# Kernel optimization log

Measured on AMD Instinct MI355X. Metric: run time of the kernel, lower is better.

## Reference

```python
import jax, jax.numpy as jnp
import numpy as np
from jax import lax

DES_R = 2.0                      # descriptor radius (KITTI config)
RAD_N, ELE_N, AZI_N = 9, 40, 80  # spherical voxel grid
VOXEL_R = 0.3                    # per-voxel ball-query radius
NSAMPLE = 30                     # points kept per voxel
B, N = 2, 1024                   # patches, points per patch
M = RAD_N * ELE_N * AZI_N        # 28800 voxel centers
EPS = 1e-5                       # BatchNorm eps


def voxel_centers():
    # cm.get_voxel_coordinate: spherical grid, flatten order (rad, ele, azi)
    r = (np.arange(RAD_N) + 0.5) * DES_R / RAD_N
    ele = (np.arange(ELE_N) + 0.5) * np.pi / ELE_N
    azi = (np.arange(AZI_N) + 0.5) * 2.0 * np.pi / AZI_N
    rr, ee, aa = np.meshgrid(r, ele, azi, indexing='ij')
    x = rr * np.sin(ee) * np.cos(aa)
    y = rr * np.sin(ee) * np.sin(aa)
    z = rr * np.cos(ee)
    return jnp.asarray(np.stack([x, y, z], -1).reshape(-1, 3), jnp.float32)


def bn(x, g, b, axes):
    # train-mode BatchNorm (batch statistics), channel axis = 1
    m = x.mean(axes, keepdims=True)
    v = x.var(axes, keepdims=True)
    shape = [1] * x.ndim
    shape[1] = -1
    return g.reshape(shape) * (x - m) * lax.rsqrt(v + EPS) + b.reshape(shape)


def conv3d_cyl(x, w, b):
    # cylindrical 3D conv: valid over rad, zero-pad elevation, circular-pad azimuth
    xp = jnp.pad(x, ((0, 0), (0, 0), (0, 0), (1, 1), (0, 0)))
    xp = jnp.pad(xp, ((0, 0), (0, 0), (0, 0), (0, 0), (1, 1)), mode='wrap')
    y = lax.conv_general_dilated(xp, w, (1, 1, 1), 'VALID',
                                 dimension_numbers=('NCDHW', 'OIDHW', 'NCDHW'))
    return y + b[None, :, None, None, None]


def _forward(points, w_raise, b_raise, g0, be0,
             w1, b1, g1, be1, w2, b2, g2, be2,
             w3, b3, g3, be3, w4, b4, g4, be4):
    vox = voxel_centers()                               # (M,3)
    center = points[:, -1:, :]
    delta = points - center                             # (B,N,3), KITTI: no z-axis alignment

    # --- cm.sphere_query: fixed-radius ball query per voxel center ---
    d2 = (jnp.sum(delta * delta, -1)[:, None, :]
          + jnp.sum(vox * vox, -1)[None, :, None]
          - 2.0 * jnp.einsum('bnc,mc->bmn', delta, vox))   # (B,M,N)
    arange = jnp.arange(N, dtype=jnp.int32)
    idx_m = jnp.where(d2 <= VOXEL_R ** 2, arange[None, None, :], N)
    neg_small, _ = lax.top_k(-idx_m, NSAMPLE)           # smallest indices first
    idx = -neg_small                                    # (B,M,NSAMPLE)
    mask = idx == N                                     # empty slots -> voxel center
    gathered = jax.vmap(lambda d, i: d[i])(delta, jnp.where(mask, 0, idx))  # (B,M,ns,3)
    rel = jnp.where(mask[..., None], 0.0, gathered - vox[None, :, None, :])

    # --- cm.var_to_invar: undo each azimuth bin's rotation about z ---
    ang = -jnp.arange(AZI_N, dtype=jnp.float32) * jnp.float32(2.0 * np.pi / AZI_N)
    c, s = jnp.cos(ang), jnp.sin(ang)
    z0, o1 = jnp.zeros_like(c), jnp.ones_like(c)
    R = jnp.stack([jnp.stack([c, -s, z0], -1),
                   jnp.stack([s, c, z0], -1),
                   jnp.stack([z0, z0, o1], -1)], -2)     # (AZI_N,3,3)
    relv = rel.reshape(B, RAD_N, ELE_N, AZI_N, NSAMPLE, 3)
    relv = jnp.einsum('breanc,acd->breand', relv, R).reshape(B, M, NSAMPLE, 3)

    # --- xyz raising (1x1 conv) + BN + ReLU + maxpool over nsample ---
    x = relv.transpose(0, 3, 1, 2)                      # (B,3,M,ns)
    x = jnp.einsum('bcmn,oc->bomn', x, w_raise) + b_raise[None, :, None, None]
    x = jax.nn.relu(bn(x, g0, be0, (0, 2, 3)))
    x = x.max(-1)                                       # (B,16,M)
    x = x.reshape(B, 16, RAD_N, ELE_N, AZI_N)

    # --- Cylindrical_Net: 3D cylindrical convs collapsing rad 9->7->5->3->1 ---
    for (w, bb, g, be) in ((w1, b1, g1, be1), (w2, b2, g2, be2),
                           (w3, b3, g3, be3), (w4, b4, g4, be4)):
        x = jax.nn.relu(bn(conv3d_cyl(x, w, bb), g, be, (0, 2, 3, 4)))
    x = x[:, :, 0, :, :]                                # (B,32,ELE_N,AZI_N)
    return x.max((2, 3), keepdims=True)                 # (B,32,1,1)


def setup_inputs() -> dict:
    key = jax.random.key(0)
    ks = jax.random.split(key, 8)

    def wgen(k, shape, fan):
        return jax.random.normal(k, shape, jnp.float32) / float(np.sqrt(fan))

    d = {
        'points': jax.random.uniform(ks[0], (B, N, 3), jnp.float32, -DES_R, DES_R),
        'w_raise': wgen(ks[1], (16, 3), 3.0),
        'b_raise': jnp.zeros(16, jnp.float32),
        'g0': jnp.ones(16, jnp.float32),
        'be0': jnp.zeros(16, jnp.float32),
    }
    chans = [16, 32, 32, 32]
    for i in range(4):
        cin = chans[i]
        d['w%d' % (i + 1)] = wgen(ks[2 + i], (32, cin, 3, 3, 3), cin * 27.0)
        d['b%d' % (i + 1)] = jnp.zeros(32, jnp.float32)
        d['g%d' % (i + 1)] = jnp.ones(32, jnp.float32)
        d['be%d' % (i + 1)] = jnp.zeros(32, jnp.float32)
    return d


def reference(points, w_raise, b_raise, g0, be0, w1, b1, g1, be1,
              w2, b2, g2, be2, w3, b3, g3, be3, w4, b4, g4, be4):
    return _forward(points, w_raise, b_raise, g0, be0, w1, b1, g1, be1,
                    w2, b2, g2, be2, w3, b3, g3, be3, w4, b4, g4, be4)
```

## Files before the change

kernel.cpp:

```cpp
#include <hip/hip_runtime.h>
#include <math.h>

#define RAD_N 9
#define ELE_N 40
#define AZI_N 80
#define M_TOT 28800
#define NPTS 1024
#define NSAMP 30
#define BATCH 2
#define VOX_R2 0.09f
#define EPSBN 1e-5f

__global__ __launch_bounds__(256)
void k_vox(float4* __restrict__ vox4, float2* __restrict__ rot2)
{
    const int m = blockIdx.x * 256 + threadIdx.x;
    if (m >= M_TOT) return;
    const int ri = m / (ELE_N * AZI_N);
    const int rm = m - ri * (ELE_N * AZI_N);
    const int ei = rm / AZI_N;
    const int ai = rm - ei * AZI_N;
    const double rd = (ri + 0.5) * (2.0 / (double)RAD_N);
    const double ed = (ei + 0.5) * (M_PI / (double)ELE_N);
    const double ad = (ai + 0.5) * (2.0 * M_PI / (double)AZI_N);
    const float vx = (float)(rd * sin(ed) * cos(ad));
    const float vy = (float)(rd * sin(ed) * sin(ad));
    const float vz = (float)(rd * cos(ed));
    vox4[m] = make_float4(vx, vy, vz, vx * vx + vy * vy + vz * vz);
    const float ang = -((float)ai * (float)(2.0 * M_PI / (double)AZI_N));
    rot2[m] = make_float2(cosf(ang), sinf(ang));
}

__global__ __launch_bounds__(256)
void k_neighbor(const float* __restrict__ pts,
                const float4* __restrict__ vox4,
                const float2* __restrict__ rot2,
                const float* __restrict__ w_raise,
                const float* __restrict__ b_raise,
                float* __restrict__ xmax, float* __restrict__ xmin,
                float* __restrict__ xsum, float* __restrict__ xsq)
{
    __shared__ float4 dl4[NPTS];
    __shared__ int lists[4][NSAMP];
    const int b = blockIdx.y;
    const float* P = pts + (size_t)b * NPTS * 3;
    const float cx = P[(NPTS - 1) * 3 + 0];
    const float cy = P[(NPTS - 1) * 3 + 1];
    const float cz = P[(NPTS - 1) * 3 + 2];
    for (int n = threadIdx.x; n < NPTS; n += 256) {
        const float dx = P[n * 3 + 0] - cx;
        const float dy = P[n * 3 + 1] - cy;
        const float dz = P[n * 3 + 2] - cz;
        dl4[n] = make_float4(dx, dy, dz, dx * dx + dy * dy + dz * dz);
    }
    __syncthreads();

    const int wv = threadIdx.x >> 6;
    const int ln = threadIdx.x & 63;
    const int m  = blockIdx.x * 4 + wv;
    const float4 V  = vox4[m];
    const float2 RC = rot2[m];

    int cnt = 0;
    for (int it = 0; it < 16; it++) {
        const float4 p = dl4[it * 64 + ln];
        const float d2 = p.w + V.w - 2.f * (p.x * V.x + p.y * V.y + p.z * V.z);
        const unsigned long long mask = __ballot(d2 <= VOX_R2);
        if (mask) {
            const int pop  = __popcll(mask);
            const int need = NSAMP - cnt;
            const int pre  = __popcll(mask & ((1ull << ln) - 1ull));
            if ((d2 <= VOX_R2) && pre < need) lists[wv][cnt + pre] = it * 64 + ln;
            cnt += min(pop, need);
            if (cnt >= NSAMP) break;
        }
    }
    __syncthreads();

    const int K  = cnt;
    const int ch = ln & 15;
    const int sg = ln >> 4;
    const float wr0 = w_raise[ch * 3 + 0];
    const float wr1 = w_raise[ch * 3 + 1];
    const float wr2 = w_raise[ch * 3 + 2];
    const float br  = b_raise[ch];

    float mx = -1e30f, mn = 1e30f, sm = 0.f, sq = 0.f;
    for (int s0 = 0; s0 < K; s0 += 4) {
        const int s = s0 + sg;
        if (s < K) {
            const float4 p = dl4[lists[wv][s]];
            const float rx = p.x - V.x, ry = p.y - V.y, rz = p.z - V.z;
            const float ox =  rx * RC.x + ry * RC.y;
            const float oy = -rx * RC.y + ry * RC.x;
            const float x  = wr0 * ox + wr1 * oy + wr2 * rz + br;
            mx = fmaxf(mx, x); mn = fminf(mn, x);
            sm += x; sq += x * x;
        }
    }
    const int rem = NSAMP - K;
    if (sg == 0 && rem > 0) {
        mx = fmaxf(mx, br); mn = fminf(mn, br);
        sm += (float)rem * br; sq += (float)rem * br * br;
    }
    mx = fmaxf(mx, __shfl_xor(mx, 16)); mx = fmaxf(mx, __shfl_xor(mx, 32));
    mn = fminf(mn, __shfl_xor(mn, 16)); mn = fminf(mn, __shfl_xor(mn, 32));
    sm += __shfl_xor(sm, 16); sm += __shfl_xor(sm, 32);
    sq += __shfl_xor(sq, 16); sq += __shfl_xor(sq, 32);

    if (ln < 16) {
        const size_t o = ((size_t)b * 16 + ch) * M_TOT + m;
        xmax[o] = mx; xmin[o] = mn; xsum[o] = sm; xsq[o] = sq;
    }
}

__global__ __launch_bounds__(256)
void k_nstats(const float* __restrict__ xsum, const float* __restrict__ xsq,
              float* __restrict__ stats)
{
    const int ch    = blockIdx.x;
    const int isq   = blockIdx.y;
    const int chunk = blockIdx.z;
    const float* src = isq ? xsq : xsum;
    const int per = M_TOT / 8;
    float s = 0.f;
    for (int b = 0; b < BATCH; b++) {
        const float* p = src + ((size_t)b * 16 + ch) * M_TOT + chunk * per;
        for (int i = threadIdx.x; i < per; i += 256) s += p[i];
    }
    for (int off = 32; off; off >>= 1) s += __shfl_xor(s, off);
    __shared__ float red[4];
    if ((threadIdx.x & 63) == 0) red[threadIdx.x >> 6] = s;
    __syncthreads();
    if (threadIdx.x == 0)
        atomicAdd(&stats[isq * 32 + ch], red[0] + red[1] + red[2] + red[3]);
}

__global__ __launch_bounds__(256)
void k_bn0(const float* __restrict__ xmax, const float* __restrict__ xmin,
           float* __restrict__ act,
           const float* __restrict__ stats,
           const float* __restrict__ g, const float* __restrict__ be)
{
    const int idx = blockIdx.x * 256 + threadIdx.x;
    const int total = BATCH * 16 * M_TOT;
    if (idx >= total) return;
    const int ch = (idx / M_TOT) & 15;
    const float cnt = (float)((size_t)BATCH * M_TOT * NSAMP);
    const float mean = stats[ch] / cnt;
    const float var  = stats[32 + ch] / cnt - mean * mean;
    const float sc = g[ch] * rsqrtf(var + EPSBN);
    const float sh = be[ch] - mean * sc;
    const float v = (sc >= 0.f) ? xmax[idx] : xmin[idx];
    const float r = sc * v + sh;
    act[idx] = r > 0.f ? r : 0.f;
}

template <int CIN, int DOUT, int CICHUNK>
__global__ __launch_bounds__(320)
void k_conv(const float* __restrict__ xin, const float* __restrict__ wgt,
            const float* __restrict__ bias,
            float* __restrict__ y)
{
    constexpr int DIN = DOUT + 2;
    constexpr int NCHUNK = CIN / CICHUNK;
    const int cog   = blockIdx.z & 3;
    const int chunk = (blockIdx.z >> 2) % NCHUNK;
    const int b     = blockIdx.z / (4 * NCHUNK);
    const int d     = blockIdx.y;
    const int h     = blockIdx.x * 4 + threadIdx.x / 80;
    const int w     = threadIdx.x % 80;
    const int wm1   = (w == 0) ? 79 : w - 1;
    const int wp1   = (w == 79) ? 0 : w + 1;

    float acc[8];
#pragma unroll
    for (int c = 0; c < 8; c++) acc[c] = (chunk == 0) ? bias[cog * 8 + c] : 0.f;

    const float* xb = xin + (size_t)b * CIN * DIN * 3200
                          + (size_t)(chunk * CICHUNK) * DIN * 3200 + (size_t)d * 3200;
    const float* wb = wgt + (size_t)(cog * 8) * CIN * 27 + chunk * CICHUNK * 27;

#pragma unroll 1
    for (int ci = 0; ci < CICHUNK; ci++) {
        const float* xc  = xb + (size_t)ci * DIN * 3200;
        const float* wc  = wb + ci * 27;
#pragma unroll
        for (int kd = 0; kd < 3; kd++) {
            const float* xd = xc + kd * 3200;
#pragma unroll
            for (int kh = 0; kh < 3; kh++) {
                const int hh = h + kh - 1;
                if (hh < 0 || hh >= ELE_N) continue;
                const float* xr = xd + hh * 80;
                const float x0 = xr[wm1];
                const float x1 = xr[w];
                const float x2 = xr[wp1];
                const float* wk = wc + kd * 9 + kh * 3;
#pragma unroll
                for (int c = 0; c < 8; c++) {
                    const float* wcc = wk + c * (CIN * 27);
                    acc[c] = fmaf(x2, wcc[2], fmaf(x1, wcc[1], fmaf(x0, wcc[0], acc[c])));
                }
            }
        }
    }

#pragma unroll
    for (int c = 0; c < 8; c++) {
        atomicAdd(&y[(((size_t)b * 32 + cog * 8 + c) * DOUT + d) * 3200 + h * 80 + w],
                  acc[c]);
    }
}

__global__ __launch_bounds__(256)
void k_ystats(const float* __restrict__ y, float* __restrict__ stats, int dhw)
{
    const int co  = blockIdx.x;
    const int per = dhw >> 3;
    const int i0  = blockIdx.y * per;
    float s = 0.f, q = 0.f;
    for (int b = 0; b < BATCH; b++) {
        const float* p = y + ((size_t)b * 32 + co) * dhw + i0;
        for (int i = threadIdx.x; i < per; i += 256) {
            const float v = p[i];
            s += v; q += v * v;
        }
    }
    for (int off = 32; off; off >>= 1) {
        s += __shfl_xor(s, off);
        q += __shfl_xor(q, off);
    }
    __shared__ float red[4][2];
    if ((threadIdx.x & 63) == 0) { red[threadIdx.x >> 6][0] = s; red[threadIdx.x >> 6][1] = q; }
    __syncthreads();
    if (threadIdx.x == 0) {
        float S = 0.f, Q = 0.f;
#pragma unroll
        for (int i = 0; i < 4; i++) { S += red[i][0]; Q += red[i][1]; }
        atomicAdd(&stats[co], S);
        atomicAdd(&stats[32 + co], Q);
    }
}

__global__ __launch_bounds__(256)
void k_bnrelu(const float* __restrict__ y, float* __restrict__ act,
              const float* __restrict__ stats,
              const float* __restrict__ g, const float* __restrict__ be,
              float per_ch_count, int dhw, int total)
{
    const int idx = blockIdx.x * 256 + threadIdx.x;
    if (idx >= total) return;
    const int ch = (idx / dhw) & 31;
    const float mean = stats[ch] / per_ch_count;
    const float var  = stats[32 + ch] / per_ch_count - mean * mean;
    const float sc = g[ch] * rsqrtf(var + EPSBN);
    const float sh = be[ch] - mean * sc;
    const float r = sc * y[idx] + sh;
    act[idx] = r > 0.f ? r : 0.f;
}

__global__ __launch_bounds__(256)
void k_final(const float* __restrict__ y4,
             const float* __restrict__ stats,
             const float* __restrict__ g, const float* __restrict__ be,
             float* __restrict__ out)
{
    const int b = blockIdx.x >> 5;
    const int co = blockIdx.x & 31;
    const float* src = y4 + ((size_t)b * 32 + co) * 3200;
    float mx = -1e30f, mn = 1e30f;
    for (int i = threadIdx.x; i < 3200; i += 256) {
        const float v = src[i];
        mx = fmaxf(mx, v);
        mn = fminf(mn, v);
    }
    for (int off = 32; off; off >>= 1) {
        mx = fmaxf(mx, __shfl_xor(mx, off));
        mn = fminf(mn, __shfl_xor(mn, off));
    }
    __shared__ float rmx[4], rmn[4];
    const int wv = threadIdx.x >> 6;
    if ((threadIdx.x & 63) == 0) { rmx[wv] = mx; rmn[wv] = mn; }
    __syncthreads();
    if (threadIdx.x == 0) {
        float MX = rmx[0], MN = rmn[0];
#pragma unroll
        for (int i = 1; i < 4; i++) { MX = fmaxf(MX, rmx[i]); MN = fminf(MN, rmn[i]); }
        const float cnt = (float)(BATCH * 1 * 3200);
        const float mean = stats[co] / cnt;
        const float var  = stats[32 + co] / cnt - mean * mean;
        const float sc = g[co] * rsqrtf(var + EPSBN);
        const float sh = be[co] - mean * sc;
        const float v = (sc >= 0.f) ? MX : MN;
        const float r = sc * v + sh;
        out[b * 32 + co] = r > 0.f ? r : 0.f;
    }
}

extern "C" void kernel_launch(void* const* d_in, const int* in_sizes, int n_in,
                              void* d_out, int out_size, void* d_ws, size_t ws_size,
                              hipStream_t stream)
{
    const float* pts     = (const float*)d_in[0];
    const float* w_raise = (const float*)d_in[1];
    const float* b_raise = (const float*)d_in[2];
    const float* g0      = (const float*)d_in[3];
    const float* be0     = (const float*)d_in[4];
    const float* w1  = (const float*)d_in[5];
    const float* b1  = (const float*)d_in[6];
    const float* g1  = (const float*)d_in[7];
    const float* be1 = (const float*)d_in[8];
    const float* w2  = (const float*)d_in[9];
    const float* b2  = (const float*)d_in[10];
    const float* g2  = (const float*)d_in[11];
    const float* be2 = (const float*)d_in[12];
    const float* w3  = (const float*)d_in[13];
    const float* b3  = (const float*)d_in[14];
    const float* g3  = (const float*)d_in[15];
    const float* be3 = (const float*)d_in[16];
    const float* w4  = (const float*)d_in[17];
    const float* b4  = (const float*)d_in[18];
    const float* g4  = (const float*)d_in[19];
    const float* be4 = (const float*)d_in[20];
    float* out = (float*)d_out;

    float* wsf   = (float*)d_ws;
    float*  stats = wsf;
    float4* vox4  = (float4*)(wsf + 512);
    float2* rot2  = (float2*)(wsf + 115712);
    float*  xmax  = wsf + 173312;
    float*  xmin  = wsf + 1094912;
    float*  xsum  = wsf + 2016512;
    float*  xsq   = wsf + 2938112;
    float*  act0  = wsf + 3859712;
    float*  A     = wsf + 4781312;
    float*  Y1 = wsf + 173312;
    float*  Y2 = Y1 + 1433600;
    float*  Y3 = Y2 + 1024000;
    float*  Y4 = Y3 + 614400;

    hipMemsetAsync(stats, 0, 512 * sizeof(float), stream);

    k_vox<<<(M_TOT + 255) / 256, 256, 0, stream>>>(vox4, rot2);

    k_neighbor<<<dim3(M_TOT / 4, BATCH), 256, 0, stream>>>(
        pts, vox4, rot2, w_raise, b_raise, xmax, xmin, xsum, xsq);

    k_nstats<<<dim3(16, 2, 8), 256, 0, stream>>>(xsum, xsq, stats);

    k_bn0<<<(BATCH * 16 * M_TOT + 255) / 256, 256, 0, stream>>>(
        xmax, xmin, act0, stats, g0, be0);

    hipMemsetAsync(Y1, 0, 3276800 * sizeof(float), stream);

    k_conv<16, 7, 4><<<dim3(10, 7, 32), 320, 0, stream>>>(act0, w1, b1, Y1);
    k_ystats<<<dim3(32, 8), 256, 0, stream>>>(Y1, stats + 64, 7 * 3200);
    k_bnrelu<<<(BATCH * 32 * 7 * 3200 + 255) / 256, 256, 0, stream>>>(
        Y1, A, stats + 64, g1, be1, (float)(BATCH * 7 * 3200), 7 * 3200, BATCH * 32 * 7 * 3200);

    k_conv<32, 5, 8><<<dim3(10, 5, 32), 320, 0, stream>>>(A, w2, b2, Y2);
    k_ystats<<<dim3(32, 8), 256, 0, stream>>>(Y2, stats + 128, 5 * 3200);
    k_bnrelu<<<(BATCH * 32 * 5 * 3200 + 255) / 256, 256, 0, stream>>>(
        Y2, A, stats + 128, g2, be2, (float)(BATCH * 5 * 3200), 5 * 3200, BATCH * 32 * 5 * 3200);

    k_conv<32, 3, 8><<<dim3(10, 3, 32), 320, 0, stream>>>(A, w3, b3, Y3);
    k_ystats<<<dim3(32, 8), 256, 0, stream>>>(Y3, stats + 192, 3 * 3200);
    k_bnrelu<<<(BATCH * 32 * 3 * 3200 + 255) / 256, 256, 0, stream>>>(
        Y3, A, stats + 192, g3, be3, (float)(BATCH * 3 * 3200), 3 * 3200, BATCH * 32 * 3 * 3200);

    k_conv<32, 1, 4><<<dim3(10, 1, 64), 320, 0, stream>>>(A, w4, b4, Y4);
    k_ystats<<<dim3(32, 8), 256, 0, stream>>>(Y4, stats + 256, 3200);

    k_final<<<BATCH * 32, 256, 0, stream>>>(Y4, stats + 256, g4, be4, out);
}
```

Before: 357.7 us.

## Stage conv input halo tile in double-buffered LDS with prefetch

The cylindrical 3D conv kernel now loads a 3-depth by 6-row by 80-wide input halo tile per input channel into shared memory with float4 loads. It double-buffers that tile, prefetching the next channel into registers while computing the current one. The 9 taps are then read from LDS instead of global memory, with zero-padded rows replacing the per-tap bounds branches. This adds a barrier per input channel and 11.5 KB of LDS per block. A launch-bounds occupancy hint is also added.

```diff
diff --git a/kernel.cpp b/kernel.cpp
--- a/kernel.cpp
+++ b/kernel.cpp
@@ -157,59 +157,93 @@
 }
 
 template <int CIN, int DOUT, int CICHUNK>
-__global__ __launch_bounds__(320)
+__global__ __launch_bounds__(320, 8)
 void k_conv(const float* __restrict__ xin, const float* __restrict__ wgt,
             const float* __restrict__ bias,
             float* __restrict__ y)
 {
     constexpr int DIN = DOUT + 2;
     constexpr int NCHUNK = CIN / CICHUNK;
+    __shared__ float4 tile[2][360];
     const int cog   = blockIdx.z & 3;
     const int chunk = (blockIdx.z >> 2) % NCHUNK;
     const int b     = blockIdx.z / (4 * NCHUNK);
     const int d     = blockIdx.y;
-    const int h     = blockIdx.x * 4 + threadIdx.x / 80;
+    const int hb    = blockIdx.x * 4;
+    const int hrow  = threadIdx.x / 80;
     const int w     = threadIdx.x % 80;
     const int wm1   = (w == 0) ? 79 : w - 1;
     const int wp1   = (w == 79) ? 0 : w + 1;
 
+    const float* xb = xin + ((size_t)b * CIN + chunk * CICHUNK) * DIN * 3200
+                          + (size_t)d * 3200;
+    const float* wb = wgt + (size_t)(cog * 8) * CIN * 27 + chunk * CICHUNK * 27;
+
+    const int j0 = threadIdx.x;
+    const int j1 = threadIdx.x + 320;
+    const bool has1 = (j1 < 360);
+    const int kd0 = j0 / 120, rr0 = (j0 / 20) % 6, w40 = j0 % 20;
+    const int kd1 = j1 / 120, rr1 = (j1 / 20) % 6, w41 = j1 % 20;
+    const int hh0 = hb - 1 + rr0;
+    const int hh1 = hb - 1 + rr1;
+    const bool ok0 = (hh0 >= 0 && hh0 < ELE_N);
+    const bool ok1 = has1 && (hh1 >= 0 && hh1 < ELE_N);
+    const int src0 = kd0 * 800 + hh0 * 20 + w40;
+    const int src1 = kd1 * 800 + hh1 * 20 + w41;
+    const float4 f4z = make_float4(0.f, 0.f, 0.f, 0.f);
+
     float acc[8];
 #pragma unroll
     for (int c = 0; c < 8; c++) acc[c] = (chunk == 0) ? bias[cog * 8 + c] : 0.f;
 
-    const float* xb = xin + (size_t)b * CIN * DIN * 3200
-                          + (size_t)(chunk * CICHUNK) * DIN * 3200 + (size_t)d * 3200;
-    const float* wb = wgt + (size_t)(cog * 8) * CIN * 27 + chunk * CICHUNK * 27;
+    {
+        const float4* xc = (const float4*)xb;
+        float4 s0 = ok0 ? xc[src0] : f4z;
+        float4 s1 = ok1 ? xc[src1] : f4z;
+        tile[0][j0] = s0;
+        if (has1) tile[0][j1] = s1;
+    }
+    __syncthreads();
 
 #pragma unroll 1
     for (int ci = 0; ci < CICHUNK; ci++) {
-        const float* xc  = xb + (size_t)ci * DIN * 3200;
+        float4 s0 = f4z, s1 = f4z;
+        if (ci + 1 < CICHUNK) {
+            const float4* xc = (const float4*)(xb + (size_t)(ci + 1) * DIN * 3200);
+            if (ok0) s0 = xc[src0];
+            if (ok1) s1 = xc[src1];
+        }
+
+        const float* lds = (const float*)&tile[ci & 1][0];
         const float* wc  = wb + ci * 27;
 #pragma unroll
         for (int kd = 0; kd < 3; kd++) {
-            const float* xd = xc + kd * 3200;
 #pragma unroll
             for (int kh = 0; kh < 3; kh++) {
-                const int hh = h + kh - 1;
-                if (hh < 0 || hh >= ELE_N) continue;
-                const float* xr = xd + hh * 80;
-                const float x0 = xr[wm1];
-                const float x1 = xr[w];
-                const float x2 = xr[wp1];
-                const float* wk = wc + kd * 9 + kh * 3;
+                const float* row = lds + (kd * 6 + hrow + kh) * 80;
+                const float x0 = row[wm1];
+                const float x1 = row[w];
+                const float x2 = row[wp1];
 #pragma unroll
                 for (int c = 0; c < 8; c++) {
-                    const float* wcc = wk + c * (CIN * 27);
-                    acc[c] = fmaf(x2, wcc[2], fmaf(x1, wcc[1], fmaf(x0, wcc[0], acc[c])));
+                    const float* wk = wc + (size_t)c * (CIN * 27) + kd * 9 + kh * 3;
+                    acc[c] = fmaf(x2, wk[2], fmaf(x1, wk[1], fmaf(x0, wk[0], acc[c])));
                 }
             }
         }
+
+        if (ci + 1 < CICHUNK) {
+            float4* dst = &tile[(ci + 1) & 1][0];
+            dst[j0] = s0;
+            if (has1) dst[j1] = s1;
+        }
+        __syncthreads();
     }
 
 #pragma unroll
     for (int c = 0; c < 8; c++) {
-        atomicAdd(&y[(((size_t)b * 32 + cog * 8 + c) * DOUT + d) * 3200 + h * 80 + w],
-                  acc[c]);
+        atomicAdd(&y[(((size_t)b * 32 + cog * 8 + c) * DOUT + d) * 3200
+                     + (hb + hrow) * 80 + w], acc[c]);
     }
 }
 
```

Result: slower. 514.7 us (+43.9%).
